# Optimization experiments

Measured on AMD Instinct MI355X. Metric: run time of the kernel, lower is better.

Reference implementation:

```python
import jax, jax.numpy as jnp
import numpy as np

IN_F, OUT_F, RANK = 4096, 4096, 1024
B, S_LEN = 4, 2048


def _dequant(data, scale, zp):
    # (int_data - zero_point) * scale, per-tensor scalar quantization
    return (data.astype(jnp.float32) - zp.astype(jnp.float32)) * scale.astype(jnp.float32)


def setup_inputs() -> dict:
    key = jax.random.key(0)
    ks = jax.random.split(key, 8)
    x = jax.random.normal(ks[0], (B, S_LEN, IN_F), dtype=jnp.float32)
    U_data = jax.random.randint(ks[1], (OUT_F, RANK), 0, 255, dtype=jnp.int32)
    S_data = jax.random.randint(ks[2], (RANK,), 0, 255, dtype=jnp.int32)
    Vh_data = jax.random.randint(ks[3], (RANK, IN_F), 0, 255, dtype=jnp.int32)
    bias = jax.random.normal(ks[4], (OUT_F,), dtype=jnp.float32)
    return {
        "x": x,
        "U_data": U_data,
        "U_scale": jnp.array([0.02], dtype=jnp.float32),
        "U_zp": jnp.array([128.0], dtype=jnp.float32),
        "S_data": S_data,
        "S_scale": jnp.array([0.05], dtype=jnp.float32),
        "S_zp": jnp.array([128.0], dtype=jnp.float32),
        "Vh_data": Vh_data,
        "Vh_scale": jnp.array([0.02], dtype=jnp.float32),
        "Vh_zp": jnp.array([128.0], dtype=jnp.float32),
        "bias": bias,
    }


def reference(x, U_data, U_scale, U_zp, S_data, S_scale, S_zp,
              Vh_data, Vh_scale, Vh_zp, bias):
    U = _dequant(U_data, U_scale, U_zp)     # [out, r]
    S = _dequant(S_data, S_scale, S_zp)     # [r]
    Vh = _dequant(Vh_data, Vh_scale, Vh_zp)  # [r, in]
    orig_shape = x.shape
    x_flat = x.reshape(-1, orig_shape[-1])  # [N, in]
    h = x_flat @ Vh.T                        # [N, r]
    h = h * S[None, :]
    y = h @ U.T                              # [N, out]
    y = y + bias
    return y.reshape(orig_shape[:-1] + (U.shape[0],))
```

## Files before the change

### kernel.cpp

```cpp
#include <hip/hip_runtime.h>
#include <stdint.h>

#define NROWS 8192
#define INF   4096
#define OUTF  4096
#define RNK   1024

typedef unsigned short u16;
typedef __attribute__((ext_vector_type(8))) short bf16x8;
typedef __attribute__((ext_vector_type(4))) float f32x4;
typedef __attribute__((ext_vector_type(8))) unsigned short u16x8;

__device__ __forceinline__ u16 f32_bf16(float f) {
  union { float f; uint32_t u; } v; v.f = f;
  return (u16)((v.u + 0x7FFF + ((v.u >> 16) & 1)) >> 16);
}


__global__ __launch_bounds__(256) void convert_x(const float* __restrict__ x,
                                                 u16* __restrict__ o) {
  int t = blockIdx.x * 256 + threadIdx.x;
  int e = t * 8;
  float4 a = *(const float4*)(x + e);
  float4 b = *(const float4*)(x + e + 4);
  u16x8 r;
  r[0] = f32_bf16(a.x); r[1] = f32_bf16(a.y); r[2] = f32_bf16(a.z); r[3] = f32_bf16(a.w);
  r[4] = f32_bf16(b.x); r[5] = f32_bf16(b.y); r[6] = f32_bf16(b.z); r[7] = f32_bf16(b.w);
  *(u16x8*)(o + e) = r;
}

__global__ __launch_bounds__(256) void dequant_vh(const int* __restrict__ vh,
                                                  const float* __restrict__ vs,
                                                  const float* __restrict__ vz,
                                                  const int* __restrict__ sd,
                                                  const float* __restrict__ ss,
                                                  const float* __restrict__ sz,
                                                  u16* __restrict__ o) {
  int t = blockIdx.x * 256 + threadIdx.x;
  int e = t * 4;
  int row = e >> 12;
  float sval = ((float)sd[row] - sz[0]) * ss[0];
  float sc = vs[0] * sval;
  float zp = vz[0];
  int4 d = *(const int4*)(vh + e);
  ushort4 r;
  r.x = f32_bf16(((float)d.x - zp) * sc);
  r.y = f32_bf16(((float)d.y - zp) * sc);
  r.z = f32_bf16(((float)d.z - zp) * sc);
  r.w = f32_bf16(((float)d.w - zp) * sc);
  *(ushort4*)(o + e) = r;
}

__global__ __launch_bounds__(256) void dequant_u(const int* __restrict__ ud,
                                                 const float* __restrict__ us,
                                                 const float* __restrict__ uz,
                                                 u16* __restrict__ o) {
  int t = blockIdx.x * 256 + threadIdx.x;
  int e = t * 4;
  float sc = us[0];
  float zp = uz[0];
  int4 d = *(const int4*)(ud + e);
  ushort4 r;
  r.x = f32_bf16(((float)d.x - zp) * sc);
  r.y = f32_bf16(((float)d.y - zp) * sc);
  r.z = f32_bf16(((float)d.z - zp) * sc);
  r.w = f32_bf16(((float)d.w - zp) * sc);
  *(ushort4*)(o + e) = r;
}


__device__ __forceinline__ void gl_lds16(const u16* g, u16* l) {
  __builtin_amdgcn_global_load_lds(
      (const __attribute__((address_space(1))) void*)g,
      (__attribute__((address_space(3))) void*)l, 16, 0, 0);
}

template <int VM> __device__ __forceinline__ void vm_wait() {
  static_assert(VM == 3 || VM == 4, "unexpected vmcnt");
  if constexpr (VM == 3) asm volatile("s_waitcnt vmcnt(3)" ::: "memory");
  if constexpr (VM == 4) asm volatile("s_waitcnt vmcnt(4)" ::: "memory");
}

template <int BN, int K, int N, bool OUT_BF16, bool ADD_BIAS>
__global__ __launch_bounds__(512, 2) void gemm8p(const u16* __restrict__ A,
                                                 const u16* __restrict__ B,
                                                 void* __restrict__ Cv,
                                                 const float* __restrict__ bias) {
  constexpr int BM = 256, BK = 64;
  constexpr int WN = BN / 4;
  constexpr int QJ = WN / 32;
  constexpr int LB = (BN == 256) ? 2 : 1;
  constexpr int NT = K / BK;
  constexpr int AH = 128 * BK;
  constexpr int BH = (BN / 2) * BK;

  __shared__ __attribute__((aligned(16))) u16 ldsA[2 * 2 * AH];
  __shared__ __attribute__((aligned(16))) u16 ldsB[2 * 2 * BH];

  const int tid  = threadIdx.x;
  const int lane = tid & 63;
  const int wave = tid >> 6;
  const int wm   = wave >> 2;
  const int wn   = wave & 3;
  const int bm   = blockIdx.y * BM;
  const int bn   = blockIdx.x * BN;

  const int srow = tid >> 3;
  const int spc  = tid & 7;
  const int sgc  = spc ^ (srow & 7);

  const u16* gA = A + (size_t)(bm + srow) * K + sgc * 8;
  const u16* gB = B + (size_t)(bn + srow) * K + sgc * 8;
  u16* lA = ldsA + srow * BK + spc * 8;
  u16* lB = ldsB + srow * BK + spc * 8;

#define STAGE_A(buf, h, kt)                                                    \
  { const u16* g_ = gA + (size_t)(h) * 128 * K + (kt);                         \
    u16* l_ = lA + ((buf) * 2 + (h)) * AH;                                     \
    gl_lds16(g_, l_);                                                          \
    gl_lds16(g_ + (size_t)64 * K, l_ + 64 * BK); }

#define STAGE_B(buf, h, kt)                                                    \
  { const u16* g_ = gB + (size_t)(h) * (BN / 2) * K + (kt);                    \
    u16* l_ = lB + ((buf) * 2 + (h)) * BH;                                     \
    gl_lds16(g_, l_);                                                          \
    if constexpr (LB == 2) gl_lds16(g_ + (size_t)64 * K, l_ + 64 * BK); }

  const int r   = lane & 15;
  const int kq  = (lane >> 4) * 8;
  const int pc0 = (((kq) >> 3) ^ (r & 7)) << 3;
  const int pc1 = (((32 + kq) >> 3) ^ (r & 7)) << 3;

  f32x4 acc[2][2][4][QJ] = {};

#define PHASE(buf, qm, qn, STAGE, VMW)                                         \
  {                                                                            \
    bf16x8 af[4][2], bfr[QJ][2];                                               \
    const u16* abase = ldsA + ((buf) * 2 + (qm)) * AH + (wm * 64 + r) * BK;    \
    _Pragma("unroll")                                                          \
    for (int i = 0; i < 4; ++i) {                                              \
      af[i][0] = *(const bf16x8*)(abase + i * 16 * BK + pc0);                  \
      af[i][1] = *(const bf16x8*)(abase + i * 16 * BK + pc1);                  \
    }                                                                          \
    const u16* bbase =                                                         \
        ldsB + ((buf) * 2 + (qn)) * BH + (wn * (WN / 2) + r) * BK;             \
    _Pragma("unroll")                                                          \
    for (int j = 0; j < QJ; ++j) {                                             \
      bfr[j][0] = *(const bf16x8*)(bbase + j * 16 * BK + pc0);                 \
      bfr[j][1] = *(const bf16x8*)(bbase + j * 16 * BK + pc1);                 \
    }                                                                          \
    STAGE;                                                                     \
    __builtin_amdgcn_sched_barrier(0);                                         \
    __builtin_amdgcn_s_barrier();                                              \
    __builtin_amdgcn_sched_barrier(0);                                         \
    __builtin_amdgcn_s_setprio(1);                                             \
    _Pragma("unroll")                                                          \
    for (int i = 0; i < 4; ++i)                                                \
      _Pragma("unroll")                                                        \
      for (int j = 0; j < QJ; ++j) {                                           \
        acc[qm][qn][i][j] = __builtin_amdgcn_mfma_f32_16x16x32_bf16(           \
            af[i][0], bfr[j][0], acc[qm][qn][i][j], 0, 0, 0);                  \
        acc[qm][qn][i][j] = __builtin_amdgcn_mfma_f32_16x16x32_bf16(           \
            af[i][1], bfr[j][1], acc[qm][qn][i][j], 0, 0, 0);                  \
      }                                                                        \
    __builtin_amdgcn_s_setprio(0);                                             \
    __builtin_amdgcn_sched_barrier(0);                                         \
    VMW;                                                                       \
    __builtin_amdgcn_s_barrier();                                              \
    __builtin_amdgcn_sched_barrier(0);                                         \
  }

  STAGE_A(0, 0, 0);
  STAGE_B(0, 0, 0);
  STAGE_B(0, 1, 0);
  STAGE_A(0, 1, 0);
  __builtin_amdgcn_sched_barrier(0);
  constexpr int KT1 = (NT > 1 ? BK : 0);
  STAGE_A(1, 0, KT1);
  STAGE_B(1, 0, KT1);
  __builtin_amdgcn_sched_barrier(0);
  vm_wait<2 + LB>();
  __builtin_amdgcn_s_barrier();
  __builtin_amdgcn_sched_barrier(0);

  for (int t = 0; t < NT; ++t) {
    const int buf  = t & 1;
    const int nbuf = buf ^ 1;
    const int kt1 = (t + 1 < NT ? t + 1 : NT - 1) * BK;
    const int kt2 = (t + 2 < NT ? t + 2 : NT - 1) * BK;
    PHASE(buf, 0, 0, STAGE_B(nbuf, 1, kt1), );
    PHASE(buf, 0, 1, STAGE_A(nbuf, 1, kt1), );
    PHASE(buf, 1, 0, STAGE_A(buf, 0, kt2), );
    PHASE(buf, 1, 1, STAGE_B(buf, 0, kt2), (vm_wait<2 + LB>()));
  }

  const int col0 = lane & 15;
  const int row0 = (lane >> 4) * 4;
#pragma unroll
  for (int qm = 0; qm < 2; ++qm)
#pragma unroll
    for (int qn = 0; qn < 2; ++qn)
#pragma unroll
      for (int j = 0; j < QJ; ++j) {
        const int gcol = bn + (qn * 4 + wn) * (WN / 2) + j * 16 + col0;
        float bv = 0.f;
        if constexpr (ADD_BIAS) bv = bias[gcol];
#pragma unroll
        for (int i = 0; i < 4; ++i)
#pragma unroll
          for (int rr = 0; rr < 4; ++rr) {
            const int grow = bm + qm * 128 + wm * 64 + i * 16 + row0 + rr;
            float v = acc[qm][qn][i][j][rr] + bv;
            if constexpr (OUT_BF16)
              ((u16*)Cv)[(size_t)grow * N + gcol] = f32_bf16(v);
            else
              ((float*)Cv)[(size_t)grow * N + gcol] = v;
          }
      }
#undef PHASE
#undef STAGE_A
#undef STAGE_B
}


extern "C" void kernel_launch(void* const* d_in, const int* in_sizes, int n_in,
                              void* d_out, int out_size, void* d_ws, size_t ws_size,
                              hipStream_t stream) {
  const float* x        = (const float*)d_in[0];
  const int*   U_data   = (const int*)d_in[1];
  const float* U_scale  = (const float*)d_in[2];
  const float* U_zp     = (const float*)d_in[3];
  const int*   S_data   = (const int*)d_in[4];
  const float* S_scale  = (const float*)d_in[5];
  const float* S_zp     = (const float*)d_in[6];
  const int*   Vh_data  = (const int*)d_in[7];
  const float* Vh_scale = (const float*)d_in[8];
  const float* Vh_zp    = (const float*)d_in[9];
  const float* bias     = (const float*)d_in[10];
  float* out = (float*)d_out;

  char* ws = (char*)d_ws;
  u16* xb  = (u16*)ws;
  u16* vhb = (u16*)(ws + (size_t)67108864);
  u16* ub  = (u16*)(ws + (size_t)67108864 + 8388608);
  u16* hb  = (u16*)(ws + (size_t)67108864 + 16777216);

  convert_x<<<NROWS * INF / (8 * 256), 256, 0, stream>>>(x, xb);
  dequant_vh<<<RNK * INF / (4 * 256), 256, 0, stream>>>(Vh_data, Vh_scale, Vh_zp,
                                                        S_data, S_scale, S_zp, vhb);
  dequant_u<<<OUTF * RNK / (4 * 256), 256, 0, stream>>>(U_data, U_scale, U_zp, ub);

  gemm8p<128, INF, RNK, true, false>
      <<<dim3(RNK / 128, NROWS / 256), 512, 0, stream>>>(xb, vhb, (void*)hb, nullptr);

  gemm8p<256, RNK, OUTF, false, true>
      <<<dim3(OUTF / 256, NROWS / 256), 512, 0, stream>>>(hb, ub, (void*)out, bias);
}
```

Measured before the change: 491.5 us.

## Reuse LDS fragments across GEMM quadrants with snake order and configurable wave grid

Replaces the 8-phase GEMM, which reloaded both A and B fragments from LDS in every quadrant phase, with a 4-phase schedule. The quadrants run in snake order (00, 01, 11, 10), so each phase loads only one new A or B fragment set and reuses the other from registers. The wave grid is now a template parameter (4x2 for the first GEMM, 2x4 for the second), and the staging order of global-to-LDS copies is reshuffled to match the new phase order. This cuts LDS read traffic and barriers per K-tile, at the cost of more live fragment registers (two B sets) and tighter correctness margins on buffer reuse timing.

```diff
diff --git a/kernel.cpp b/kernel.cpp
--- a/kernel.cpp
+++ b/kernel.cpp
@@ -81,14 +81,16 @@
   if constexpr (VM == 4) asm volatile("s_waitcnt vmcnt(4)" ::: "memory");
 }
 
-template <int BN, int K, int N, bool OUT_BF16, bool ADD_BIAS>
-__global__ __launch_bounds__(512, 2) void gemm8p(const u16* __restrict__ A,
+template <int BN, int WM, int WN, int K, int N, bool OUT_BF16, bool ADD_BIAS>
+__global__ __launch_bounds__(512, 2) void gemm4p(const u16* __restrict__ A,
                                                  const u16* __restrict__ B,
                                                  void* __restrict__ Cv,
                                                  const float* __restrict__ bias) {
   constexpr int BM = 256, BK = 64;
-  constexpr int WN = BN / 4;
-  constexpr int QJ = WN / 32;
+  constexpr int AR = 128 / WM;
+  constexpr int BC = (BN / 2) / WN;
+  constexpr int AI = AR / 16;
+  constexpr int BJ = BC / 16;
   constexpr int LB = (BN == 256) ? 2 : 1;
   constexpr int NT = K / BK;
   constexpr int AH = 128 * BK;
@@ -100,8 +102,8 @@
   const int tid  = threadIdx.x;
   const int lane = tid & 63;
   const int wave = tid >> 6;
-  const int wm   = wave >> 2;
-  const int wn   = wave & 3;
+  const int wn   = wave % WN;
+  const int wm   = wave / WN;
   const int bm   = blockIdx.y * BM;
   const int bn   = blockIdx.x * BN;
 
@@ -131,95 +133,120 @@
   const int pc0 = (((kq) >> 3) ^ (r & 7)) << 3;
   const int pc1 = (((32 + kq) >> 3) ^ (r & 7)) << 3;
 
-  f32x4 acc[2][2][4][QJ] = {};
-
-#define PHASE(buf, qm, qn, STAGE, VMW)                                         \
-  {                                                                            \
-    bf16x8 af[4][2], bfr[QJ][2];                                               \
-    const u16* abase = ldsA + ((buf) * 2 + (qm)) * AH + (wm * 64 + r) * BK;    \
+  f32x4 acc[2][2][AI][BJ] = {};
+  bf16x8 af[AI][2];
+  bf16x8 bf0[BJ][2];
+  bf16x8 bf1[BJ][2];
+
+#define LOAD_A(buf, ih)                                                        \
+  { const u16* ab = ldsA + ((buf) * 2 + (ih)) * AH + (wm * AR + r) * BK;       \
     _Pragma("unroll")                                                          \
-    for (int i = 0; i < 4; ++i) {                                              \
-      af[i][0] = *(const bf16x8*)(abase + i * 16 * BK + pc0);                  \
-      af[i][1] = *(const bf16x8*)(abase + i * 16 * BK + pc1);                  \
-    }                                                                          \
-    const u16* bbase =                                                         \
-        ldsB + ((buf) * 2 + (qn)) * BH + (wn * (WN / 2) + r) * BK;             \
+    for (int i = 0; i < AI; ++i) {                                             \
+      af[i][0] = *(const bf16x8*)(ab + i * 16 * BK + pc0);                     \
+      af[i][1] = *(const bf16x8*)(ab + i * 16 * BK + pc1);                     \
+    } }
+
+#define LOAD_B(dst, buf, jh)                                                   \
+  { const u16* bb = ldsB + ((buf) * 2 + (jh)) * BH + (wn * BC + r) * BK;       \
     _Pragma("unroll")                                                          \
-    for (int j = 0; j < QJ; ++j) {                                             \
-      bfr[j][0] = *(const bf16x8*)(bbase + j * 16 * BK + pc0);                 \
-      bfr[j][1] = *(const bf16x8*)(bbase + j * 16 * BK + pc1);                 \
-    }                                                                          \
-    STAGE;                                                                     \
-    __builtin_amdgcn_sched_barrier(0);                                         \
-    __builtin_amdgcn_s_barrier();                                              \
-    __builtin_amdgcn_sched_barrier(0);                                         \
-    __builtin_amdgcn_s_setprio(1);                                             \
+    for (int j = 0; j < BJ; ++j) {                                             \
+      dst[j][0] = *(const bf16x8*)(bb + j * 16 * BK + pc0);                    \
+      dst[j][1] = *(const bf16x8*)(bb + j * 16 * BK + pc1);                    \
+    } }
+
+#define MFMA_Q(ih, jh, bsrc)                                                   \
+  _Pragma("unroll")                                                            \
+  for (int i = 0; i < AI; ++i)                                                 \
     _Pragma("unroll")                                                          \
-    for (int i = 0; i < 4; ++i)                                                \
-      _Pragma("unroll")                                                        \
-      for (int j = 0; j < QJ; ++j) {                                           \
-        acc[qm][qn][i][j] = __builtin_amdgcn_mfma_f32_16x16x32_bf16(           \
-            af[i][0], bfr[j][0], acc[qm][qn][i][j], 0, 0, 0);                  \
-        acc[qm][qn][i][j] = __builtin_amdgcn_mfma_f32_16x16x32_bf16(           \
-            af[i][1], bfr[j][1], acc[qm][qn][i][j], 0, 0, 0);                  \
-      }                                                                        \
-    __builtin_amdgcn_s_setprio(0);                                             \
-    __builtin_amdgcn_sched_barrier(0);                                         \
-    VMW;                                                                       \
-    __builtin_amdgcn_s_barrier();                                              \
-    __builtin_amdgcn_sched_barrier(0);                                         \
-  }
+    for (int j = 0; j < BJ; ++j) {                                             \
+      acc[ih][jh][i][j] = __builtin_amdgcn_mfma_f32_16x16x32_bf16(             \
+          af[i][0], bsrc[j][0], acc[ih][jh][i][j], 0, 0, 0);                   \
+      acc[ih][jh][i][j] = __builtin_amdgcn_mfma_f32_16x16x32_bf16(             \
+          af[i][1], bsrc[j][1], acc[ih][jh][i][j], 0, 0, 0);                   \
+    }
+
+#define SB  __builtin_amdgcn_sched_barrier(0)
+#define BAR __builtin_amdgcn_s_barrier()
+#define PRIO1 __builtin_amdgcn_s_setprio(1)
+#define PRIO0 __builtin_amdgcn_s_setprio(0)
 
   STAGE_A(0, 0, 0);
   STAGE_B(0, 0, 0);
   STAGE_B(0, 1, 0);
   STAGE_A(0, 1, 0);
-  __builtin_amdgcn_sched_barrier(0);
+  SB;
   constexpr int KT1 = (NT > 1 ? BK : 0);
   STAGE_A(1, 0, KT1);
-  STAGE_B(1, 0, KT1);
-  __builtin_amdgcn_sched_barrier(0);
+  STAGE_B(1, 1, KT1);
+  SB;
   vm_wait<2 + LB>();
-  __builtin_amdgcn_s_barrier();
-  __builtin_amdgcn_sched_barrier(0);
+  BAR;
+  SB;
 
   for (int t = 0; t < NT; ++t) {
     const int buf  = t & 1;
     const int nbuf = buf ^ 1;
     const int kt1 = (t + 1 < NT ? t + 1 : NT - 1) * BK;
     const int kt2 = (t + 2 < NT ? t + 2 : NT - 1) * BK;
-    PHASE(buf, 0, 0, STAGE_B(nbuf, 1, kt1), );
-    PHASE(buf, 0, 1, STAGE_A(nbuf, 1, kt1), );
-    PHASE(buf, 1, 0, STAGE_A(buf, 0, kt2), );
-    PHASE(buf, 1, 1, STAGE_B(buf, 0, kt2), (vm_wait<2 + LB>()));
+
+    LOAD_A(buf, 0); LOAD_B(bf0, buf, 0);
+    STAGE_A(nbuf, 1, kt1);
+    SB; BAR; SB; PRIO1;
+    MFMA_Q(0, 0, bf0);
+    PRIO0; SB; BAR; SB;
+
+    LOAD_B(bf1, buf, 1);
+    STAGE_B(nbuf, 0, kt1);
+    SB; BAR; SB; PRIO1;
+    MFMA_Q(0, 1, bf1);
+    PRIO0; SB; BAR; SB;
+
+    LOAD_A(buf, 1);
+    STAGE_A(buf, 0, kt2);
+    SB; BAR; SB; PRIO1;
+    MFMA_Q(1, 1, bf1);
+    PRIO0; SB; BAR; SB;
+
+    STAGE_B(buf, 1, kt2);
+    SB; BAR; SB; PRIO1;
+    MFMA_Q(1, 0, bf0);
+    PRIO0; SB;
+    vm_wait<2 + LB>();
+    BAR; SB;
   }
 
   const int col0 = lane & 15;
   const int row0 = (lane >> 4) * 4;
 #pragma unroll
-  for (int qm = 0; qm < 2; ++qm)
-#pragma unroll
-    for (int qn = 0; qn < 2; ++qn)
-#pragma unroll
-      for (int j = 0; j < QJ; ++j) {
-        const int gcol = bn + (qn * 4 + wn) * (WN / 2) + j * 16 + col0;
+  for (int ih = 0; ih < 2; ++ih)
+#pragma unroll
+    for (int jh = 0; jh < 2; ++jh)
+#pragma unroll
+      for (int j = 0; j < BJ; ++j) {
+        const int gcol = bn + jh * (BN / 2) + wn * BC + j * 16 + col0;
         float bv = 0.f;
         if constexpr (ADD_BIAS) bv = bias[gcol];
 #pragma unroll
-        for (int i = 0; i < 4; ++i)
+        for (int i = 0; i < AI; ++i)
 #pragma unroll
           for (int rr = 0; rr < 4; ++rr) {
-            const int grow = bm + qm * 128 + wm * 64 + i * 16 + row0 + rr;
-            float v = acc[qm][qn][i][j][rr] + bv;
+            const int grow = bm + ih * 128 + wm * AR + i * 16 + row0 + rr;
+            float v = acc[ih][jh][i][j][rr] + bv;
             if constexpr (OUT_BF16)
               ((u16*)Cv)[(size_t)grow * N + gcol] = f32_bf16(v);
             else
               ((float*)Cv)[(size_t)grow * N + gcol] = v;
           }
       }
-#undef PHASE
+#undef MFMA_Q
+#undef LOAD_A
+#undef LOAD_B
 #undef STAGE_A
 #undef STAGE_B
+#undef SB
+#undef BAR
+#undef PRIO1
+#undef PRIO0
 }
 
 
@@ -250,9 +277,9 @@
                                                         S_data, S_scale, S_zp, vhb);
   dequant_u<<<OUTF * RNK / (4 * 256), 256, 0, stream>>>(U_data, U_scale, U_zp, ub);
 
-  gemm8p<128, INF, RNK, true, false>
+  gemm4p<128, 4, 2, INF, RNK, true, false>
       <<<dim3(RNK / 128, NROWS / 256), 512, 0, stream>>>(xb, vhb, (void*)hb, nullptr);
 
-  gemm8p<256, RNK, OUTF, false, true>
+  gemm4p<256, 2, 4, RNK, OUTF, false, true>
       <<<dim3(OUTF / 256, NROWS / 256), 512, 0, stream>>>(hb, ub, (void*)out, bias);
 }
```

After: 447.8 us. 1.1x faster.
